# Optimization experiments

Measured on AMD Instinct MI355X. Metric: run time of the kernel, lower is better.

The kernel has to match this reference:

```python
import jax, jax.numpy as jnp
import numpy as np

B, T, HID = 2, 1024, 2048
NH, NKV, HD = 16, 4, 128
L, INTER = 4, 5632
EPS = 1e-6


def _rope_tables(key):
    inv_freq = 1.0 / (10000.0 ** (jnp.arange(0, HD, 2, dtype=jnp.float32) / HD))  # [HD/2]
    pos = jnp.arange(T, dtype=jnp.float32)
    freqs = pos[:, None] * inv_freq[None, :]          # [T, HD/2]
    emb = jnp.concatenate([freqs, freqs], axis=-1)    # [T, HD]
    cos = jnp.broadcast_to(jnp.cos(emb)[None], (B, T, HD))
    sin = jnp.broadcast_to(jnp.sin(emb)[None], (B, T, HD))
    return cos, sin


def setup_inputs() -> dict:
    key = jax.random.key(0)
    ks = jax.random.split(key, 12)
    std = 0.02
    cos, sin = _rope_tables(key)
    return {
        "hidden_states": jax.random.normal(ks[0], (B, T, HID), jnp.float32),
        "cos": cos,
        "sin": sin,
        "qw": jax.random.normal(ks[1], (L, NH * HD, HID), jnp.float32) * std,
        "qb": jnp.zeros((L, NH * HD), jnp.float32),
        "kw": jax.random.normal(ks[2], (L, NKV * HD, HID), jnp.float32) * std,
        "kb": jnp.zeros((L, NKV * HD), jnp.float32),
        "vw": jax.random.normal(ks[3], (L, NKV * HD, HID), jnp.float32) * std,
        "vb": jnp.zeros((L, NKV * HD), jnp.float32),
        "ow": jax.random.normal(ks[4], (L, HID, NH * HD), jnp.float32) * std,
        "gatew": jax.random.normal(ks[5], (L, INTER, HID), jnp.float32) * std,
        "upw": jax.random.normal(ks[6], (L, INTER, HID), jnp.float32) * std,
        "downw": jax.random.normal(ks[7], (L, HID, INTER), jnp.float32) * std,
        "ln1w": jnp.ones((L, HID), jnp.float32),
        "ln2w": jnp.ones((L, HID), jnp.float32),
        "normw": jnp.ones((HID,), jnp.float32),
    }


def _rmsnorm(x, w):
    xf = x.astype(jnp.float32)
    var = jnp.mean(xf * xf, axis=-1, keepdims=True)
    return (w * (xf * jax.lax.rsqrt(var + EPS))).astype(x.dtype)


def _rotate_half(x):
    x1, x2 = x[..., : HD // 2], x[..., HD // 2:]
    return jnp.concatenate([-x2, x1], axis=-1)


def _layer(x, cos, sin, mask, qw, qb, kw, kb, vw, vb, ow, gw, uw, dw, l1, l2):
    # --- attention (PreNorm) ---
    h = _rmsnorm(x, l1)
    q = (h @ qw.T + qb).reshape(B, T, NH, HD).transpose(0, 2, 1, 3)    # [B,NH,T,D]
    k = (h @ kw.T + kb).reshape(B, T, NKV, HD).transpose(0, 2, 1, 3)   # [B,NKV,T,D]
    v = (h @ vw.T + vb).reshape(B, T, NKV, HD).transpose(0, 2, 1, 3)
    c, s = cos[:, None], sin[:, None]                                  # [B,1,T,D]
    q = q * c + _rotate_half(q) * s
    k = k * c + _rotate_half(k) * s
    rep = NH // NKV
    k = jnp.repeat(k, rep, axis=1)                                     # GQA repeat_kv
    v = jnp.repeat(v, rep, axis=1)
    scores = jnp.einsum("bhqd,bhkd->bhqk", q, k) / (HD ** 0.5) + mask
    attn = jax.nn.softmax(scores.astype(jnp.float32), axis=-1).astype(q.dtype)
    ao = jnp.einsum("bhqk,bhkd->bhqd", attn, v)
    ao = ao.transpose(0, 2, 1, 3).reshape(B, T, NH * HD) @ ow.T
    x = x + ao
    # --- SwiGLU MLP (PreNorm) ---
    h = _rmsnorm(x, l2)
    x = x + (jax.nn.silu(h @ gw.T) * (h @ uw.T)) @ dw.T
    return x


def reference(hidden_states, cos, sin, qw, qb, kw, kb, vw, vb, ow,
              gatew, upw, downw, ln1w, ln2w, normw):
    min_val = jnp.finfo(hidden_states.dtype).min
    qpos = jnp.arange(T)
    mask = jnp.where(qpos[None, :] > qpos[:, None], min_val, 0.0).astype(hidden_states.dtype)
    mask = mask[None, None]  # [1,1,T,T]
    x = hidden_states
    for i in range(L):
        x = _layer(x, cos, sin, mask, qw[i], qb[i], kw[i], kb[i], vw[i], vb[i],
                   ow[i], gatew[i], upw[i], downw[i], ln1w[i], ln2w[i])
    return _rmsnorm(x, normw)
```

## Files before the change

kernel.cpp:

```cpp
#include <hip/hip_runtime.h>


typedef __attribute__((ext_vector_type(8))) __bf16 bf16x8;
typedef __attribute__((ext_vector_type(4))) float f32x4;
typedef __attribute__((ext_vector_type(4))) unsigned short u16x4;

#define DEV __device__ __forceinline__
#define BARRIER() asm volatile("s_barrier" ::: "memory")

#define NTOK 2048
#define HIDDIM 2048
#define NHEADS 16
#define NKVH 4
#define HDIM 128
#define KVDIM 512
#define INTERDIM 5632

DEV unsigned short f2bf(float f) {
  union { float f; unsigned u; } a; a.f = f;
  unsigned r = a.u + 0x7fffu + ((a.u >> 16) & 1u);
  return (unsigned short)(r >> 16);
}
DEV float bf2f(unsigned short h) {
  union { unsigned u; float f; } a; a.u = ((unsigned)h) << 16;
  return a.f;
}
DEV unsigned short f2h(float f) {
  union { _Float16 h; unsigned short u; } c; c.h = (_Float16)f; return c.u;
}
DEV float h2f(unsigned short u) {
  union { unsigned short u; _Float16 h; } c; c.u = u; return (float)c.h;
}
DEV void gload_lds16(const void* g, void* l) {
  __builtin_amdgcn_global_load_lds(
      (const __attribute__((address_space(1))) unsigned int*)(g),
      (__attribute__((address_space(3))) unsigned int*)(l), 16, 0, 0);
}

__global__ __launch_bounds__(256) void cvt_kernel(
    const float* __restrict__ in, unsigned short* __restrict__ out, int n8) {
  const int i = blockIdx.x * 256 + threadIdx.x;
  if (i >= n8) return;
  const f32x4* p = reinterpret_cast<const f32x4*>(in) + (size_t)i * 2;
  const f32x4 a = p[0], b = p[1];
  bf16x8 o;
  o[0] = (__bf16)a.x; o[1] = (__bf16)a.y; o[2] = (__bf16)a.z; o[3] = (__bf16)a.w;
  o[4] = (__bf16)b.x; o[5] = (__bf16)b.y; o[6] = (__bf16)b.z; o[7] = (__bf16)b.w;
  *reinterpret_cast<bf16x8*>(out + (size_t)i * 8) = o;
}

__global__ __launch_bounds__(256) void cvt_gu(
    const float* __restrict__ gw, const float* __restrict__ uw,
    unsigned short* __restrict__ out) {
  const int i = blockIdx.x * 256 + threadIdx.x;
  const int row = i >> 8, g8 = i & 255;
  const int t = row >> 8, sub = row & 255;
  const float* src = (sub < 128)
                         ? gw + (size_t)(t * 128 + sub) * 2048
                         : uw + (size_t)(t * 128 + sub - 128) * 2048;
  const f32x4* p = reinterpret_cast<const f32x4*>(src) + (size_t)g8 * 2;
  const f32x4 a = p[0], b = p[1];
  bf16x8 o;
  o[0] = (__bf16)a.x; o[1] = (__bf16)a.y; o[2] = (__bf16)a.z; o[3] = (__bf16)a.w;
  o[4] = (__bf16)b.x; o[5] = (__bf16)b.y; o[6] = (__bf16)b.z; o[7] = (__bf16)b.w;
  *reinterpret_cast<bf16x8*>(out + (size_t)row * 2048 + g8 * 8) = o;
}

template <int OUTF32>
__global__ __launch_bounds__(256) void rmsnorm_kernel(
    const float* __restrict__ x, const float* __restrict__ w,
    void* __restrict__ outp) {
  const int row = blockIdx.x, tid = threadIdx.x;
  const int lane = tid & 63, wave = tid >> 6;
  const float* xr = x + (size_t)row * HIDDIM;
  f32x4 v0 = *reinterpret_cast<const f32x4*>(xr + tid * 4);
  f32x4 v1 = *reinterpret_cast<const f32x4*>(xr + 1024 + tid * 4);
  float ss = v0.x * v0.x + v0.y * v0.y + v0.z * v0.z + v0.w * v0.w +
             v1.x * v1.x + v1.y * v1.y + v1.z * v1.z + v1.w * v1.w;
#pragma unroll
  for (int off = 1; off < 64; off <<= 1) ss += __shfl_xor(ss, off, 64);
  __shared__ float red[4];
  if (lane == 0) red[wave] = ss;
  __syncthreads();
  ss = red[0] + red[1] + red[2] + red[3];
  const float rs = rsqrtf(ss * (1.0f / 2048.0f) + 1e-6f);
  f32x4 w0 = *reinterpret_cast<const f32x4*>(w + tid * 4);
  f32x4 w1 = *reinterpret_cast<const f32x4*>(w + 1024 + tid * 4);
  if (OUTF32) {
    float* o = (float*)outp + (size_t)row * HIDDIM;
    f32x4 o0, o1;
    o0.x = v0.x * rs * w0.x; o0.y = v0.y * rs * w0.y;
    o0.z = v0.z * rs * w0.z; o0.w = v0.w * rs * w0.w;
    o1.x = v1.x * rs * w1.x; o1.y = v1.y * rs * w1.y;
    o1.z = v1.z * rs * w1.z; o1.w = v1.w * rs * w1.w;
    *reinterpret_cast<f32x4*>(o + tid * 4) = o0;
    *reinterpret_cast<f32x4*>(o + 1024 + tid * 4) = o1;
  } else {
    unsigned short* o = (unsigned short*)outp + (size_t)row * HIDDIM;
    u16x4 p0, p1;
    p0.x = f2bf(v0.x * rs * w0.x); p0.y = f2bf(v0.y * rs * w0.y);
    p0.z = f2bf(v0.z * rs * w0.z); p0.w = f2bf(v0.w * rs * w0.w);
    p1.x = f2bf(v1.x * rs * w1.x); p1.y = f2bf(v1.y * rs * w1.y);
    p1.z = f2bf(v1.z * rs * w1.z); p1.w = f2bf(v1.w * rs * w1.w);
    *reinterpret_cast<u16x4*>(o + tid * 4) = p0;
    *reinterpret_cast<u16x4*>(o + 1024 + tid * 4) = p1;
  }
}

template <int KS, int OUTF32>
__global__ __launch_bounds__(256) void reduce_rms(
    float* __restrict__ x, const unsigned short* __restrict__ p, size_t zs,
    const float* __restrict__ w, void* __restrict__ outp) {
  const int row = blockIdx.x, tid = threadIdx.x;
  const int lane = tid & 63, wave = tid >> 6;
  float* xr = x + (size_t)row * HIDDIM;
  f32x4 v0 = *reinterpret_cast<const f32x4*>(xr + tid * 4);
  f32x4 v1 = *reinterpret_cast<const f32x4*>(xr + 1024 + tid * 4);
#pragma unroll
  for (int s = 0; s < KS; ++s) {
    const unsigned short* pr = p + (size_t)s * zs + (size_t)row * HIDDIM;
    u16x4 a = *reinterpret_cast<const u16x4*>(pr + tid * 4);
    u16x4 b = *reinterpret_cast<const u16x4*>(pr + 1024 + tid * 4);
    v0.x += bf2f(a.x); v0.y += bf2f(a.y); v0.z += bf2f(a.z); v0.w += bf2f(a.w);
    v1.x += bf2f(b.x); v1.y += bf2f(b.y); v1.z += bf2f(b.z); v1.w += bf2f(b.w);
  }
  *reinterpret_cast<f32x4*>(xr + tid * 4) = v0;
  *reinterpret_cast<f32x4*>(xr + 1024 + tid * 4) = v1;
  float ss = v0.x * v0.x + v0.y * v0.y + v0.z * v0.z + v0.w * v0.w +
             v1.x * v1.x + v1.y * v1.y + v1.z * v1.z + v1.w * v1.w;
#pragma unroll
  for (int off = 1; off < 64; off <<= 1) ss += __shfl_xor(ss, off, 64);
  __shared__ float red[4];
  if (lane == 0) red[wave] = ss;
  __syncthreads();
  ss = red[0] + red[1] + red[2] + red[3];
  const float rs = rsqrtf(ss * (1.0f / 2048.0f) + 1e-6f);
  f32x4 w0 = *reinterpret_cast<const f32x4*>(w + tid * 4);
  f32x4 w1 = *reinterpret_cast<const f32x4*>(w + 1024 + tid * 4);
  if (OUTF32) {
    float* o = (float*)outp + (size_t)row * HIDDIM;
    f32x4 o0, o1;
    o0.x = v0.x * rs * w0.x; o0.y = v0.y * rs * w0.y;
    o0.z = v0.z * rs * w0.z; o0.w = v0.w * rs * w0.w;
    o1.x = v1.x * rs * w1.x; o1.y = v1.y * rs * w1.y;
    o1.z = v1.z * rs * w1.z; o1.w = v1.w * rs * w1.w;
    *reinterpret_cast<f32x4*>(o + tid * 4) = o0;
    *reinterpret_cast<f32x4*>(o + 1024 + tid * 4) = o1;
  } else {
    unsigned short* o = (unsigned short*)outp + (size_t)row * HIDDIM;
    u16x4 p0, p1;
    p0.x = f2bf(v0.x * rs * w0.x); p0.y = f2bf(v0.y * rs * w0.y);
    p0.z = f2bf(v0.z * rs * w0.z); p0.w = f2bf(v0.w * rs * w0.w);
    p1.x = f2bf(v1.x * rs * w1.x); p1.y = f2bf(v1.y * rs * w1.y);
    p1.z = f2bf(v1.z * rs * w1.z); p1.w = f2bf(v1.w * rs * w1.w);
    *reinterpret_cast<u16x4*>(o + tid * 4) = p0;
    *reinterpret_cast<u16x4*>(o + 1024 + tid * 4) = p1;
  }
}

template <int MB>
DEV void mfma16(const bf16x8 (&aF)[4], const bf16x8 (&bF)[4],
                f32x4 (&acc)[8][4]) {
#pragma unroll
  for (int ni = 0; ni < 4; ++ni)
#pragma unroll
    for (int mi = 0; mi < 4; ++mi)
      acc[MB + mi][ni] = __builtin_amdgcn_mfma_f32_16x16x32_bf16(
          aF[mi], bF[ni], acc[MB + mi][ni], 0, 0, 0);
}

__global__ __launch_bounds__(512, 2) void gemm8p(
    const unsigned short* __restrict__ A, const unsigned short* __restrict__ W,
    unsigned short* __restrict__ outp, int K, int ldo, int kt_split,
    int kt_tot, size_t zstride) {
  __shared__ unsigned short lds[65536];
  const int tid = threadIdx.x, lane = tid & 63, wave = tid >> 6;
  const int fr = lane & 15, lq = lane >> 4;
  const int wm = wave >> 2, wn = wave & 3;

  int bx = blockIdx.x, by = blockIdx.y;
  {
    const int nbx = gridDim.x, nwg = nbx * gridDim.y;
    const int lin = by * nbx + bx, cpx = nwg >> 3;
    const int swz = (lin & 7) * cpx + (lin >> 3);
    bx = swz % nbx; by = swz / nbx;
  }
  const int m0 = by * 256, n0 = bx * 256;
  const int bz = blockIdx.z;
  const int t0 = bz * kt_split;
  int NT = kt_tot - t0; if (NT > kt_split) NT = kt_split;

  const int u0 = tid, u1 = tid + 512;
  const int r0s = u0 >> 3, r1s = u1 >> 3;
  const size_t off0 = (size_t)r0s * K + (size_t)((((u0 & 7) ^ (r0s & 7))) << 3);
  const size_t off1 = (size_t)r1s * K + (size_t)((((u1 & 7) ^ (r1s & 7))) << 3);
  const unsigned short* gb0 = A + (size_t)(m0)*K + (size_t)t0 * 64;
  const unsigned short* gb1 = A + (size_t)(m0 + 128) * K + (size_t)t0 * 64;
  const unsigned short* gb2 = W + (size_t)(n0)*K + (size_t)t0 * 64;
  const unsigned short* gb3 = W + (size_t)(n0 + 128) * K + (size_t)t0 * 64;

#define STAGE(h_, tt_, b_)                                                    \
  do {                                                                        \
    const unsigned short* _g =                                                \
        ((h_) == 0 ? gb0 : (h_) == 1 ? gb1 : (h_) == 2 ? gb2 : gb3) +         \
        (size_t)(tt_)*64;                                                     \
    unsigned short* _l = &lds[(b_)*32768 + (h_)*8192 + wave * 512];           \
    gload_lds16(_g + off0, _l);                                               \
    gload_lds16(_g + off1, _l + 4096);                                        \
  } while (0)

  const int e0 = lq ^ (fr & 7);
  const int cbA = wm * 8192;
  const int cbB = (2 + (wn >> 1)) * 8192;
  const int rB0 = (wn & 1) * 64 + fr;

#define LDA(mi_, ks_, c_)                                                     \
  (*reinterpret_cast<const bf16x8*>(                                          \
      &lds[(c_)*32768 + cbA + ((mi_)*16 + fr) * 64 + ((e0 ^ ((ks_)*4)) << 3)]))
#define LDB(ni_, ks_, c_)                                                     \
  (*reinterpret_cast<const bf16x8*>(                                          \
      &lds[(c_)*32768 + cbB + (rB0 + (ni_)*16) * 64 + ((e0 ^ ((ks_)*4)) << 3)]))

  f32x4 acc[8][4] = {};
  bf16x8 aF[4], bF[4];

  STAGE(0, 0, 0); STAGE(1, 0, 0); STAGE(2, 0, 0); STAGE(3, 0, 0);

  for (int t = 0; t < NT; ++t) {
    const int c = t & 1;
    if (t + 1 < NT) {
      STAGE(0, t + 1, c ^ 1);
      STAGE(2, t + 1, c ^ 1);
      asm volatile("s_waitcnt vmcnt(4)" ::: "memory");
    } else {
      asm volatile("s_waitcnt vmcnt(0)" ::: "memory");
    }
    BARRIER();

    bF[0] = LDB(0, 0, c); bF[1] = LDB(1, 0, c);
    bF[2] = LDB(2, 0, c); bF[3] = LDB(3, 0, c);
    aF[0] = LDA(0, 0, c); aF[1] = LDA(1, 0, c);
    aF[2] = LDA(2, 0, c); aF[3] = LDA(3, 0, c);
    if (t + 1 < NT) { STAGE(1, t + 1, c ^ 1); STAGE(3, t + 1, c ^ 1); }
    BARRIER();
    __builtin_amdgcn_s_setprio(1);
    mfma16<0>(aF, bF, acc);
    __builtin_amdgcn_s_setprio(0);
    __builtin_amdgcn_sched_barrier(0);
    BARRIER();

    aF[0] = LDA(4, 0, c); aF[1] = LDA(5, 0, c);
    aF[2] = LDA(6, 0, c); aF[3] = LDA(7, 0, c);
    BARRIER();
    __builtin_amdgcn_s_setprio(1);
    mfma16<4>(aF, bF, acc);
    __builtin_amdgcn_s_setprio(0);
    __builtin_amdgcn_sched_barrier(0);
    BARRIER();

    bF[0] = LDB(0, 1, c); bF[1] = LDB(1, 1, c);
    bF[2] = LDB(2, 1, c); bF[3] = LDB(3, 1, c);
    aF[0] = LDA(0, 1, c); aF[1] = LDA(1, 1, c);
    aF[2] = LDA(2, 1, c); aF[3] = LDA(3, 1, c);
    BARRIER();
    __builtin_amdgcn_s_setprio(1);
    mfma16<0>(aF, bF, acc);
    __builtin_amdgcn_s_setprio(0);
    __builtin_amdgcn_sched_barrier(0);
    BARRIER();

    aF[0] = LDA(4, 1, c); aF[1] = LDA(5, 1, c);
    aF[2] = LDA(6, 1, c); aF[3] = LDA(7, 1, c);
    BARRIER();
    __builtin_amdgcn_s_setprio(1);
    mfma16<4>(aF, bF, acc);
    __builtin_amdgcn_s_setprio(0);
    __builtin_amdgcn_sched_barrier(0);
    BARRIER();
  }

  const int r0 = lq * 4;
#pragma unroll
  for (int mi = 0; mi < 8; ++mi)
#pragma unroll
    for (int ni = 0; ni < 4; ++ni)
#pragma unroll
      for (int r = 0; r < 4; ++r) {
        const int gm = m0 + wm * 128 + mi * 16 + r0 + r;
        const int gn = n0 + wn * 64 + ni * 16 + fr;
        outp[(size_t)bz * zstride + (size_t)gm * ldo + gn] =
            f2bf(acc[mi][ni][r]);
      }
#undef STAGE
#undef LDA
#undef LDB
}

__global__ __launch_bounds__(512, 2) void gemm_gu(
    const unsigned short* __restrict__ A, const unsigned short* __restrict__ W,
    unsigned short* __restrict__ act) {
  __shared__ unsigned short lds[65536];
  const int tid = threadIdx.x, lane = tid & 63, wave = tid >> 6;
  const int fr = lane & 15, lq = lane >> 4;
  const int wm = wave >> 2, wn = wave & 3;
  const int K = 2048;

  int bx = blockIdx.x, by = blockIdx.y;
  {
    const int nbx = gridDim.x, nwg = nbx * gridDim.y;
    const int lin = by * nbx + bx, cpx = nwg >> 3;
    const int swz = (lin & 7) * cpx + (lin >> 3);
    bx = swz % nbx; by = swz / nbx;
  }
  const int m0 = by * 256, n0 = bx * 256;

  const int u0 = tid, u1 = tid + 512;
  const int r0s = u0 >> 3, r1s = u1 >> 3;
  const size_t off0 = (size_t)r0s * K + (size_t)((((u0 & 7) ^ (r0s & 7))) << 3);
  const size_t off1 = (size_t)r1s * K + (size_t)((((u1 & 7) ^ (r1s & 7))) << 3);
  const unsigned short* gb0 = A + (size_t)(m0)*K;
  const unsigned short* gb1 = A + (size_t)(m0 + 128) * K;
  const unsigned short* gb2 = W + (size_t)(n0)*K;
  const unsigned short* gb3 = W + (size_t)(n0 + 128) * K;

#define STAGE(h_, tt_, b_)                                                    \
  do {                                                                        \
    const unsigned short* _g =                                                \
        ((h_) == 0 ? gb0 : (h_) == 1 ? gb1 : (h_) == 2 ? gb2 : gb3) +         \
        (size_t)(tt_)*64;                                                     \
    unsigned short* _l = &lds[(b_)*32768 + (h_)*8192 + wave * 512];           \
    gload_lds16(_g + off0, _l);                                               \
    gload_lds16(_g + off1, _l + 4096);                                        \
  } while (0)

  const int e0 = lq ^ (fr & 7);
  const int cbA = wm * 8192;
  const int cbB = (2 + (wn >> 1)) * 8192;
  const int rB0 = (wn & 1) * 64 + fr;

#define LDA(mi_, ks_, c_)                                                     \
  (*reinterpret_cast<const bf16x8*>(                                          \
      &lds[(c_)*32768 + cbA + ((mi_)*16 + fr) * 64 + ((e0 ^ ((ks_)*4)) << 3)]))
#define LDB(ni_, ks_, c_)                                                     \
  (*reinterpret_cast<const bf16x8*>(                                          \
      &lds[(c_)*32768 + cbB + (rB0 + (ni_)*16) * 64 + ((e0 ^ ((ks_)*4)) << 3)]))

  f32x4 acc[8][4] = {};
  bf16x8 aF[4], bF[4];

  STAGE(0, 0, 0); STAGE(1, 0, 0); STAGE(2, 0, 0); STAGE(3, 0, 0);

  for (int t = 0; t < 32; ++t) {
    const int c = t & 1;
    if (t + 1 < 32) {
      STAGE(0, t + 1, c ^ 1);
      STAGE(2, t + 1, c ^ 1);
      asm volatile("s_waitcnt vmcnt(4)" ::: "memory");
    } else {
      asm volatile("s_waitcnt vmcnt(0)" ::: "memory");
    }
    BARRIER();
    bF[0] = LDB(0, 0, c); bF[1] = LDB(1, 0, c);
    bF[2] = LDB(2, 0, c); bF[3] = LDB(3, 0, c);
    aF[0] = LDA(0, 0, c); aF[1] = LDA(1, 0, c);
    aF[2] = LDA(2, 0, c); aF[3] = LDA(3, 0, c);
    if (t + 1 < 32) { STAGE(1, t + 1, c ^ 1); STAGE(3, t + 1, c ^ 1); }
    BARRIER();
    __builtin_amdgcn_s_setprio(1);
    mfma16<0>(aF, bF, acc);
    __builtin_amdgcn_s_setprio(0);
    __builtin_amdgcn_sched_barrier(0);
    BARRIER();
    aF[0] = LDA(4, 0, c); aF[1] = LDA(5, 0, c);
    aF[2] = LDA(6, 0, c); aF[3] = LDA(7, 0, c);
    BARRIER();
    __builtin_amdgcn_s_setprio(1);
    mfma16<4>(aF, bF, acc);
    __builtin_amdgcn_s_setprio(0);
    __builtin_amdgcn_sched_barrier(0);
    BARRIER();
    bF[0] = LDB(0, 1, c); bF[1] = LDB(1, 1, c);
    bF[2] = LDB(2, 1, c); bF[3] = LDB(3, 1, c);
    aF[0] = LDA(0, 1, c); aF[1] = LDA(1, 1, c);
    aF[2] = LDA(2, 1, c); aF[3] = LDA(3, 1, c);
    BARRIER();
    __builtin_amdgcn_s_setprio(1);
    mfma16<0>(aF, bF, acc);
    __builtin_amdgcn_s_setprio(0);
    __builtin_amdgcn_sched_barrier(0);
    BARRIER();
    aF[0] = LDA(4, 1, c); aF[1] = LDA(5, 1, c);
    aF[2] = LDA(6, 1, c); aF[3] = LDA(7, 1, c);
    BARRIER();
    __builtin_amdgcn_s_setprio(1);
    mfma16<4>(aF, bF, acc);
    __builtin_amdgcn_s_setprio(0);
    __builtin_amdgcn_sched_barrier(0);
    BARRIER();
  }

  float* fl = reinterpret_cast<float*>(lds);
  const int r0 = lq * 4;
  __syncthreads();
  if (wn < 2) {
#pragma unroll
    for (int mi = 0; mi < 8; ++mi)
#pragma unroll
      for (int ni = 0; ni < 4; ++ni)
#pragma unroll
        for (int r = 0; r < 4; ++r)
          fl[wm * 16384 + (mi * 16 + r0 + r) * 128 + wn * 64 + ni * 16 + fr] =
              acc[mi][ni][r];
  }
  __syncthreads();
  if (wn >= 2) {
    const int wnu = wn - 2;
#pragma unroll
    for (int mi = 0; mi < 8; ++mi)
#pragma unroll
      for (int ni = 0; ni < 4; ++ni)
#pragma unroll
        for (int r = 0; r < 4; ++r) {
          const int mrow = mi * 16 + r0 + r;
          const float g =
              fl[wm * 16384 + mrow * 128 + wnu * 64 + ni * 16 + fr];
          const float s = g / (1.f + __expf(-g));
          const int gm = m0 + wm * 128 + mrow;
          const int ic = (n0 >> 1) + wnu * 64 + ni * 16 + fr;
          act[(size_t)gm * INTERDIM + ic] = f2bf(s * acc[mi][ni][r]);
        }
  }
#undef STAGE
#undef LDA
#undef LDB
}

__global__ __launch_bounds__(512, 2) void gemm_qk(
    const unsigned short* __restrict__ q, const unsigned short* __restrict__ k,
    unsigned short* __restrict__ s) {
  __shared__ unsigned short lds[65536];
  const int tid = threadIdx.x, lane = tid & 63, wave = tid >> 6;
  const int fr = lane & 15, lq = lane >> 4;
  const int wm = wave >> 2, wn = wave & 3;

  int bx = blockIdx.x, by = blockIdx.y;
  {
    const int nbx = gridDim.x, nwg = nbx * gridDim.y;
    const int lin = by * nbx + bx, cpx = nwg >> 3;
    const int swz = (lin & 7) * cpx + (lin >> 3);
    bx = swz % nbx; by = swz / nbx;
  }
  if (bx > by) return;
  const int z = blockIdx.z, b = z >> 4, h = z & 15, kvh = h >> 2;
  const unsigned short* A = q + (size_t)b * 1024 * HIDDIM + h * HDIM;
  const unsigned short* W = k + (size_t)b * 1024 * KVDIM + kvh * HDIM;
  unsigned short* outp = s + (size_t)z * 1048576;
  const int m0 = by * 256, n0 = bx * 256;

  const int u0 = tid, u1 = tid + 512;
  const int r0s = u0 >> 3, r1s = u1 >> 3;
  const int c0 = ((u0 & 7) ^ (r0s & 7)) << 3, c1 = ((u1 & 7) ^ (r1s & 7)) << 3;
  const size_t offA0 = (size_t)r0s * HIDDIM + c0;
  const size_t offA1 = (size_t)r1s * HIDDIM + c1;
  const size_t offW0 = (size_t)r0s * KVDIM + c0;
  const size_t offW1 = (size_t)r1s * KVDIM + c1;
  const unsigned short* gb0 = A + (size_t)m0 * HIDDIM;
  const unsigned short* gb1 = A + (size_t)(m0 + 128) * HIDDIM;
  const unsigned short* gb2 = W + (size_t)n0 * KVDIM;
  const unsigned short* gb3 = W + (size_t)(n0 + 128) * KVDIM;

#define QSTAGE(h_, tt_, b_)                                                   \
  do {                                                                        \
    const unsigned short* _g =                                                \
        ((h_) == 0 ? gb0 : (h_) == 1 ? gb1 : (h_) == 2 ? gb2 : gb3) +         \
        (size_t)(tt_)*64;                                                     \
    const size_t _o0 = (h_) < 2 ? offA0 : offW0;                              \
    const size_t _o1 = (h_) < 2 ? offA1 : offW1;                              \
    unsigned short* _l = &lds[(b_)*32768 + (h_)*8192 + wave * 512];           \
    gload_lds16(_g + _o0, _l);                                                \
    gload_lds16(_g + _o1, _l + 4096);                                         \
  } while (0)

  const int e0 = lq ^ (fr & 7);
  const int cbA = wm * 8192;
  const int cbB = (2 + (wn >> 1)) * 8192;
  const int rB0 = (wn & 1) * 64 + fr;

#define QLDA(mi_, ks_, c_)                                                    \
  (*reinterpret_cast<const bf16x8*>(                                          \
      &lds[(c_)*32768 + cbA + ((mi_)*16 + fr) * 64 + ((e0 ^ ((ks_)*4)) << 3)]))
#define QLDB(ni_, ks_, c_)                                                    \
  (*reinterpret_cast<const bf16x8*>(                                          \
      &lds[(c_)*32768 + cbB + (rB0 + (ni_)*16) * 64 + ((e0 ^ ((ks_)*4)) << 3)]))

  f32x4 acc[8][4] = {};
  bf16x8 aF[4], bF[4];

  QSTAGE(0, 0, 0); QSTAGE(1, 0, 0); QSTAGE(2, 0, 0); QSTAGE(3, 0, 0);

  for (int t = 0; t < 2; ++t) {
    const int c = t & 1;
    if (t == 0) {
      QSTAGE(0, 1, 1); QSTAGE(2, 1, 1);
      asm volatile("s_waitcnt vmcnt(4)" ::: "memory");
    } else {
      asm volatile("s_waitcnt vmcnt(0)" ::: "memory");
    }
    BARRIER();
    bF[0] = QLDB(0, 0, c); bF[1] = QLDB(1, 0, c);
    bF[2] = QLDB(2, 0, c); bF[3] = QLDB(3, 0, c);
    aF[0] = QLDA(0, 0, c); aF[1] = QLDA(1, 0, c);
    aF[2] = QLDA(2, 0, c); aF[3] = QLDA(3, 0, c);
    if (t == 0) { QSTAGE(1, 1, 1); QSTAGE(3, 1, 1); }
    BARRIER();
    __builtin_amdgcn_s_setprio(1);
    mfma16<0>(aF, bF, acc);
    __builtin_amdgcn_s_setprio(0);
    __builtin_amdgcn_sched_barrier(0);
    BARRIER();
    aF[0] = QLDA(4, 0, c); aF[1] = QLDA(5, 0, c);
    aF[2] = QLDA(6, 0, c); aF[3] = QLDA(7, 0, c);
    BARRIER();
    __builtin_amdgcn_s_setprio(1);
    mfma16<4>(aF, bF, acc);
    __builtin_amdgcn_s_setprio(0);
    __builtin_amdgcn_sched_barrier(0);
    BARRIER();
    bF[0] = QLDB(0, 1, c); bF[1] = QLDB(1, 1, c);
    bF[2] = QLDB(2, 1, c); bF[3] = QLDB(3, 1, c);
    aF[0] = QLDA(0, 1, c); aF[1] = QLDA(1, 1, c);
    aF[2] = QLDA(2, 1, c); aF[3] = QLDA(3, 1, c);
    BARRIER();
    __builtin_amdgcn_s_setprio(1);
    mfma16<0>(aF, bF, acc);
    __builtin_amdgcn_s_setprio(0);
    __builtin_amdgcn_sched_barrier(0);
    BARRIER();
    aF[0] = QLDA(4, 1, c); aF[1] = QLDA(5, 1, c);
    aF[2] = QLDA(6, 1, c); aF[3] = QLDA(7, 1, c);
    BARRIER();
    __builtin_amdgcn_s_setprio(1);
    mfma16<4>(aF, bF, acc);
    __builtin_amdgcn_s_setprio(0);
    __builtin_amdgcn_sched_barrier(0);
    BARRIER();
  }

  const float scale = 0.08838834764831845f;
  const int r0 = lq * 4;
#pragma unroll
  for (int mi = 0; mi < 8; ++mi)
#pragma unroll
    for (int ni = 0; ni < 4; ++ni)
#pragma unroll
      for (int r = 0; r < 4; ++r) {
        const int gm = m0 + wm * 128 + mi * 16 + r0 + r;
        const int gn = n0 + wn * 64 + ni * 16 + fr;
        outp[(size_t)gm * 1024 + gn] = f2h(acc[mi][ni][r] * scale);
      }
#undef QSTAGE
#undef QLDA
#undef QLDB
}

__global__ __launch_bounds__(256) void softmax_rows(unsigned short* __restrict__ s) {
  const int row = blockIdx.x, tid = threadIdx.x;
  const int lane = tid & 63, wave = tid >> 6;
  const int qv = row & 1023;
  const int nact = ((qv >> 8) + 1) << 8;
  unsigned short* r = s + (size_t)row * 1024;
  const int col = tid * 4;
  const bool act = (col < nact);
  float v[4];
  if (act) {
    u16x4 raw = *reinterpret_cast<const u16x4*>(r + col);
#pragma unroll
    for (int j = 0; j < 4; ++j)
      v[j] = (col + j <= qv) ? h2f(((unsigned short*)&raw)[j]) : -1e30f;
  } else {
#pragma unroll
    for (int j = 0; j < 4; ++j) v[j] = -1e30f;
  }
  float mx = fmaxf(fmaxf(v[0], v[1]), fmaxf(v[2], v[3]));
#pragma unroll
  for (int off = 1; off < 64; off <<= 1) mx = fmaxf(mx, __shfl_xor(mx, off, 64));
  __shared__ float redm[4], reds[4];
  if (lane == 0) redm[wave] = mx;
  __syncthreads();
  const float M = fmaxf(fmaxf(redm[0], redm[1]), fmaxf(redm[2], redm[3]));
  float e[4], ts = 0.f;
#pragma unroll
  for (int j = 0; j < 4; ++j) {
    e[j] = (act && col + j <= qv) ? __expf(v[j] - M) : 0.f;
    ts += e[j];
  }
#pragma unroll
  for (int off = 1; off < 64; off <<= 1) ts += __shfl_xor(ts, off, 64);
  if (lane == 0) reds[wave] = ts;
  __syncthreads();
  const float inv = 1.f / (reds[0] + reds[1] + reds[2] + reds[3]);
  if (act) {
    u16x4 o;
    o.x = f2bf(e[0] * inv); o.y = f2bf(e[1] * inv);
    o.z = f2bf(e[2] * inv); o.w = f2bf(e[3] * inv);
    *reinterpret_cast<u16x4*>(r + col) = o;
  }
}

__global__ __launch_bounds__(256, 2) void gemm_pv(
    const unsigned short* __restrict__ p, const unsigned short* __restrict__ vt,
    unsigned short* __restrict__ ao) {
  __shared__ unsigned short lds[40960];
  const int tid = threadIdx.x, lane = tid & 63, wave = tid >> 6;
  const int fr = lane & 15, lq = lane >> 4;
  const int bxn = blockIdx.x, by = blockIdx.y, z = blockIdx.z;
  const int b = z >> 4, h = z & 15, kvh = h >> 2;
  const int m0p = by * 256, n0 = bxn * 64;
  const int NT = by * 4 + 4;

  const unsigned short* A = p + (size_t)z * 1048576 + (size_t)m0p * 1024;
  const unsigned short* W =
      vt + ((size_t)(b * 4 + kvh) * 128 + n0) * 1024;

#define PVSTAGE(tt_, c_)                                                      \
  do {                                                                        \
    _Pragma("unroll")                                                         \
    for (int j = 0; j < 8; ++j) {                                             \
      const int u = wave * 512 + j * 64 + lane;                               \
      const int rw = u >> 3;                                                  \
      gload_lds16(A + (size_t)rw * 1024 + (((u & 7) ^ (rw & 7)) << 3) +       \
                      (size_t)(tt_)*64,                                       \
                  &lds[(c_)*20480 + wave * 4096 + j * 512]);                  \
    }                                                                         \
    _Pragma("unroll")                                                         \
    for (int j = 0; j < 2; ++j) {                                             \
      const int u = wave * 128 + j * 64 + lane;                               \
      const int rw = u >> 3;                                                  \
      gload_lds16(W + (size_t)rw * 1024 + (((u & 7) ^ (rw & 7)) << 3) +       \
                      (size_t)(tt_)*64,                                       \
                  &lds[(c_)*20480 + 16384 + wave * 1024 + j * 512]);          \
    }                                                                         \
  } while (0)

  const int e0 = lq ^ (fr & 7);
#define PVLDA(mi_, ks_, c_)                                                   \
  (*reinterpret_cast<const bf16x8*>(                                          \
      &lds[(c_)*20480 + (wave * 64 + (mi_)*16 + fr) * 64 +                    \
           ((e0 ^ ((ks_)*4)) << 3)]))
#define PVLDB(ni_, ks_, c_)                                                   \
  (*reinterpret_cast<const bf16x8*>(                                          \
      &lds[(c_)*20480 + 16384 + ((ni_)*16 + fr) * 64 +                        \
           ((e0 ^ ((ks_)*4)) << 3)]))

  f32x4 acc[4][4] = {};
  bf16x8 aF[4], bF[4];

  PVSTAGE(0, 0);

  for (int t = 0; t < NT; ++t) {
    const int c = t & 1;
    if (t + 1 < NT) {
      PVSTAGE(t + 1, c ^ 1);
      asm volatile("s_waitcnt vmcnt(10)" ::: "memory");
    } else {
      asm volatile("s_waitcnt vmcnt(0)" ::: "memory");
    }
    BARRIER();
#pragma unroll
    for (int ks = 0; ks < 2; ++ks) {
      bF[0] = PVLDB(0, ks, c); bF[1] = PVLDB(1, ks, c);
      bF[2] = PVLDB(2, ks, c); bF[3] = PVLDB(3, ks, c);
      aF[0] = PVLDA(0, ks, c); aF[1] = PVLDA(1, ks, c);
      aF[2] = PVLDA(2, ks, c); aF[3] = PVLDA(3, ks, c);
      BARRIER();
      __builtin_amdgcn_s_setprio(1);
#pragma unroll
      for (int ni = 0; ni < 4; ++ni)
#pragma unroll
        for (int mi = 0; mi < 4; ++mi)
          acc[mi][ni] = __builtin_amdgcn_mfma_f32_16x16x32_bf16(
              aF[mi], bF[ni], acc[mi][ni], 0, 0, 0);
      __builtin_amdgcn_s_setprio(0);
      __builtin_amdgcn_sched_barrier(0);
      BARRIER();
    }
  }

  const int r0 = lq * 4;
#pragma unroll
  for (int mi = 0; mi < 4; ++mi)
#pragma unroll
    for (int ni = 0; ni < 4; ++ni)
#pragma unroll
      for (int r = 0; r < 4; ++r) {
        const int gm = m0p + wave * 64 + mi * 16 + r0 + r;
        const int gn = n0 + ni * 16 + fr;
        ao[(size_t)(b * 1024 + gm) * HIDDIM + h * HDIM + gn] =
            f2bf(acc[mi][ni][r]);
      }
#undef PVSTAGE
#undef PVLDA
#undef PVLDB
}

__global__ __launch_bounds__(256) void reduce_qkv(
    const unsigned short* __restrict__ p, const float* __restrict__ qb,
    const float* __restrict__ kb, const float* __restrict__ vb,
    const float* __restrict__ cosb, const float* __restrict__ sinb,
    unsigned short* __restrict__ qo, unsigned short* __restrict__ ko,
    unsigned short* __restrict__ vto) {
  const int i = blockIdx.x * 256 + threadIdx.x;
  const int row = i / 768, c4 = (i - row * 768) * 4;
  const unsigned short* p0 = p + (size_t)row * 3072;
  const unsigned short* p1 = p + 6291456 + (size_t)row * 3072;
  const u16x4 a0 = *reinterpret_cast<const u16x4*>(p0 + c4);
  const u16x4 a1 = *reinterpret_cast<const u16x4*>(p1 + c4);
  f32x4 s;
  s.x = bf2f(a0.x) + bf2f(a1.x); s.y = bf2f(a0.y) + bf2f(a1.y);
  s.z = bf2f(a0.z) + bf2f(a1.z); s.w = bf2f(a0.w) + bf2f(a1.w);
  if (c4 < 2560) {
    const float* bias; unsigned short* out; int d, ldo;
    if (c4 < 2048) { bias = qb; out = qo; d = c4;        ldo = HIDDIM; }
    else           { bias = kb; out = ko; d = c4 - 2048; ldo = KVDIM; }
    const int dd = d & 127;
    const bool lohalf = (dd < 64);
    const int pc = lohalf ? c4 + 64 : c4 - 64;
    const int pd = lohalf ? d + 64 : d - 64;
    const u16x4 b0 = *reinterpret_cast<const u16x4*>(p0 + pc);
    const u16x4 b1 = *reinterpret_cast<const u16x4*>(p1 + pc);
    f32x4 sp;
    sp.x = bf2f(b0.x) + bf2f(b1.x); sp.y = bf2f(b0.y) + bf2f(b1.y);
    sp.z = bf2f(b0.z) + bf2f(b1.z); sp.w = bf2f(b0.w) + bf2f(b1.w);
    const f32x4 bv = *reinterpret_cast<const f32x4*>(bias + d);
    const f32x4 bp = *reinterpret_cast<const f32x4*>(bias + pd);
    const f32x4 cv = *reinterpret_cast<const f32x4*>(cosb + (size_t)row * 128 + dd);
    const f32x4 sv = *reinterpret_cast<const f32x4*>(sinb + (size_t)row * 128 + dd);
    const f32x4 xv = s + bv, pv = sp + bp;
    f32x4 o;
    if (lohalf) o = xv * cv - pv * sv;
    else        o = xv * cv + pv * sv;
    u16x4 ob;
    ob.x = f2bf(o.x); ob.y = f2bf(o.y); ob.z = f2bf(o.z); ob.w = f2bf(o.w);
    *reinterpret_cast<u16x4*>(out + (size_t)row * ldo + d) = ob;
  } else {
    const int d = c4 - 2560;
    const int kvh = d >> 7, dd = d & 127;
    const int b = row >> 10, t = row & 1023;
    const f32x4 bv = *reinterpret_cast<const f32x4*>(vb + d);
    const f32x4 o = s + bv;
    unsigned short* vr =
        vto + ((size_t)(b * 4 + kvh) * 128 + dd) * 1024 + t;
    vr[0] = f2bf(o.x); vr[1024] = f2bf(o.y);
    vr[2048] = f2bf(o.z); vr[3072] = f2bf(o.w);
  }
}

extern "C" void kernel_launch(void* const* d_in, const int* in_sizes, int n_in,
                              void* d_out, int out_size, void* d_ws,
                              size_t ws_size, hipStream_t stream) {
  (void)in_sizes; (void)n_in; (void)out_size; (void)ws_size;
  const float* hidden = (const float*)d_in[0];
  const float* cosb  = (const float*)d_in[1];
  const float* sinb  = (const float*)d_in[2];
  const float* qw    = (const float*)d_in[3];
  const float* qbias = (const float*)d_in[4];
  const float* kw    = (const float*)d_in[5];
  const float* kbias = (const float*)d_in[6];
  const float* vw    = (const float*)d_in[7];
  const float* vbias = (const float*)d_in[8];
  const float* ow    = (const float*)d_in[9];
  const float* gw    = (const float*)d_in[10];
  const float* uw    = (const float*)d_in[11];
  const float* dw    = (const float*)d_in[12];
  const float* ln1   = (const float*)d_in[13];
  const float* ln2   = (const float*)d_in[14];
  const float* normw = (const float*)d_in[15];

  char* ws = (char*)d_ws;
  float* x               = (float*)ws;
  unsigned short* hbuf   = (unsigned short*)(ws + 16777216);
  unsigned short* qbuf   = (unsigned short*)(ws + 25165824);
  unsigned short* kbuf   = (unsigned short*)(ws + 33554432);
  unsigned short* vtbuf  = (unsigned short*)(ws + 35651584);
  unsigned short* aobuf  = (unsigned short*)(ws + 39845888);
  unsigned short* actbuf = (unsigned short*)(ws + 71303168);
  unsigned short* wcvt   = (unsigned short*)(ws + 94371840);
  unsigned short* pbQKV = (unsigned short*)(ws + 37748736);
  unsigned short* sbuf = (unsigned short*)(ws + 48234496);
  unsigned short* pbO = (unsigned short*)(ws + 48234496);
  unsigned short* wgu = (unsigned short*)(ws + 25165824);
  unsigned short* pbD = (unsigned short*)(ws + 25165824);

  unsigned short* wq16 = wcvt;
  unsigned short* wk16 = wcvt + 4194304;
  unsigned short* wv16 = wcvt + 5242880;
  unsigned short* ow16 = wcvt;

  hipMemcpyAsync(x, hidden, (size_t)NTOK * HIDDIM * 4,
                 hipMemcpyDeviceToDevice, stream);
  rmsnorm_kernel<0><<<NTOK, 256, 0, stream>>>(x, ln1, hbuf);

  for (int l = 0; l < 4; ++l) {
    const float* qw_l = qw + (size_t)l * 2048 * 2048;
    const float* qb_l = qbias + (size_t)l * 2048;
    const float* kw_l = kw + (size_t)l * 512 * 2048;
    const float* kb_l = kbias + (size_t)l * 512;
    const float* vw_l = vw + (size_t)l * 512 * 2048;
    const float* vb_l = vbias + (size_t)l * 512;
    const float* ow_l = ow + (size_t)l * 2048 * 2048;
    const float* gw_l = gw + (size_t)l * 5632 * 2048;
    const float* uw_l = uw + (size_t)l * 5632 * 2048;
    const float* dw_l = dw + (size_t)l * 2048 * 5632;

    cvt_kernel<<<2048, 256, 0, stream>>>(qw_l, wq16, 524288);
    cvt_kernel<<<512, 256, 0, stream>>>(kw_l, wk16, 131072);
    cvt_kernel<<<512, 256, 0, stream>>>(vw_l, wv16, 131072);
    gemm8p<<<dim3(12, 8, 2), 512, 0, stream>>>(
        hbuf, wcvt, pbQKV, 2048, 3072, 16, 32, (size_t)6291456);
    reduce_qkv<<<6144, 256, 0, stream>>>(pbQKV, qb_l, kb_l, vb_l, cosb, sinb,
                                         qbuf, kbuf, vtbuf);

    gemm_qk<<<dim3(4, 4, 32), 512, 0, stream>>>(qbuf, kbuf, sbuf);
    softmax_rows<<<32768, 256, 0, stream>>>(sbuf);
    gemm_pv<<<dim3(2, 4, 32), 256, 0, stream>>>(sbuf, vtbuf, aobuf);

    cvt_kernel<<<2048, 256, 0, stream>>>(ow_l, ow16, 524288);
    gemm8p<<<dim3(8, 8, 2), 512, 0, stream>>>(
        aobuf, ow16, pbO, 2048, 2048, 16, 32, (size_t)4194304);
    reduce_rms<2, 0><<<NTOK, 256, 0, stream>>>(x, pbO, (size_t)4194304,
                                               ln2 + l * 2048, hbuf);

    cvt_gu<<<11264, 256, 0, stream>>>(gw_l, uw_l, wgu);
    gemm_gu<<<dim3(44, 8), 512, 0, stream>>>(hbuf, wgu, actbuf);

    cvt_kernel<<<5632, 256, 0, stream>>>(dw_l, wcvt, 1441792);
    gemm8p<<<dim3(8, 8, 3), 512, 0, stream>>>(
        actbuf, wcvt, pbD, 5632, 2048, 30, 88, (size_t)4194304);
    if (l < 3) {
      reduce_rms<3, 0><<<NTOK, 256, 0, stream>>>(
          x, pbD, (size_t)4194304, ln1 + (l + 1) * 2048, hbuf);
    } else {
      reduce_rms<3, 1><<<NTOK, 256, 0, stream>>>(x, pbD, (size_t)4194304,
                                                 normw, d_out);
    }
  }
}
```

Before: 1.695 ms.

## Restructure GEMMs into 16-wave blocks with 64x64 wave tiles and K-step 32

Replaces the 8-wave GEMM kernels, which used 128x64 wave tiles, K-step 64, XOR-swizzled LDS and a 128KB double buffer, with 1024-thread kernels. In the new kernels each of 16 waves computes a 64x64 tile, using a single K-step of 32 and a 64KB unswizzled double buffer. The fused gate/up epilogue now stages each wave row in turn through the smaller LDS. Split-K factors also change: the O projection and down projection move to 4-way split, with matching reduce kernels. The aim is more latency hiding from more waves per tile and less LDS per block, at the cost of lower per-wave register reuse, more barriers per unit of work and more split-K partial traffic.

```diff
diff --git a/kernel.cpp b/kernel.cpp
--- a/kernel.cpp
+++ b/kernel.cpp
@@ -10,10 +10,8 @@
 
 #define NTOK 2048
 #define HIDDIM 2048
-#define NHEADS 16
-#define NKVH 4
+#define KVDIM 512
 #define HDIM 128
-#define KVDIM 512
 #define INTERDIM 5632
 
 DEV unsigned short f2bf(float f) {
@@ -158,22 +156,75 @@
   }
 }
 
-template <int MB>
-DEV void mfma16(const bf16x8 (&aF)[4], const bf16x8 (&bF)[4],
-                f32x4 (&acc)[8][4]) {
-#pragma unroll
-  for (int ni = 0; ni < 4; ++ni)
-#pragma unroll
-    for (int mi = 0; mi < 4; ++mi)
-      acc[MB + mi][ni] = __builtin_amdgcn_mfma_f32_16x16x32_bf16(
-          aF[mi], bF[ni], acc[MB + mi][ni], 0, 0, 0);
-}
-
-__global__ __launch_bounds__(512, 2) void gemm8p(
+struct G16Setup {
+  const unsigned short* srcp0;
+  const unsigned short* srcp1;
+  int ldsc0, ldsc1;
+};
+
+DEV G16Setup g16_setup(const unsigned short* A, const unsigned short* W,
+                       int K, int m0, int n0, int t0, int wave, int lane) {
+  const int c0 = wave * 2, c1 = wave * 2 + 1;
+  const int rA = lane >> 2, cg = (lane & 3) * 8;
+  G16Setup s;
+  const unsigned short* gb[4] = {
+      A + (size_t)m0 * K, A + (size_t)(m0 + 128) * K,
+      W + (size_t)n0 * K, W + (size_t)(n0 + 128) * K};
+  s.srcp0 = gb[c0 >> 3] + (size_t)((c0 & 7) * 16 + rA) * K + cg +
+            (size_t)t0 * 32;
+  s.srcp1 = gb[c1 >> 3] + (size_t)((c1 & 7) * 16 + rA) * K + cg +
+            (size_t)t0 * 32;
+  s.ldsc0 = c0 * 512;
+  s.ldsc1 = c1 * 512;
+  return s;
+}
+
+#define G16STAGE(st_, tt_, c_)                                                \
+  do {                                                                        \
+    gload_lds16(st_.srcp0 + (size_t)(tt_)*32, &lds[(c_)*16384 + st_.ldsc0]);  \
+    gload_lds16(st_.srcp1 + (size_t)(tt_)*32, &lds[(c_)*16384 + st_.ldsc1]);  \
+  } while (0)
+
+#define G16LDA(mi_, c_)                                                       \
+  (*reinterpret_cast<const bf16x8*>(                                          \
+      &lds[(c_)*16384 + (wm >> 1) * 4096 +                                    \
+           (((wm & 1) * 64) + (mi_)*16 + fr) * 32 + lq * 8]))
+#define G16LDB(ni_, c_)                                                       \
+  (*reinterpret_cast<const bf16x8*>(                                          \
+      &lds[(c_)*16384 + (2 + (wn >> 1)) * 4096 +                              \
+           (((wn & 1) * 64) + (ni_)*16 + fr) * 32 + lq * 8]))
+
+#define G16KLOOP(NT_)                                                         \
+  G16STAGE(st, 0, 0);                                                         \
+  for (int t = 0; t < (NT_); ++t) {                                           \
+    const int c = t & 1;                                                      \
+    if (t + 1 < (NT_)) {                                                      \
+      G16STAGE(st, t + 1, c ^ 1);                                             \
+      asm volatile("s_waitcnt vmcnt(2)" ::: "memory");                        \
+    } else {                                                                  \
+      asm volatile("s_waitcnt vmcnt(0)" ::: "memory");                        \
+    }                                                                         \
+    BARRIER();                                                                \
+    bf16x8 aF[4], bF[4];                                                      \
+    bF[0] = G16LDB(0, c); bF[1] = G16LDB(1, c);                               \
+    bF[2] = G16LDB(2, c); bF[3] = G16LDB(3, c);                               \
+    aF[0] = G16LDA(0, c); aF[1] = G16LDA(1, c);                               \
+    aF[2] = G16LDA(2, c); aF[3] = G16LDA(3, c);                               \
+    __builtin_amdgcn_s_setprio(1);                                            \
+    _Pragma("unroll") for (int ni = 0; ni < 4; ++ni)                          \
+        _Pragma("unroll") for (int mi = 0; mi < 4; ++mi)                      \
+            acc[mi][ni] = __builtin_amdgcn_mfma_f32_16x16x32_bf16(            \
+                aF[mi], bF[ni], acc[mi][ni], 0, 0, 0);                        \
+    __builtin_amdgcn_s_setprio(0);                                            \
+    __builtin_amdgcn_sched_barrier(0);                                        \
+    BARRIER();                                                                \
+  }
+
+__global__ __launch_bounds__(1024) void gemm16w(
     const unsigned short* __restrict__ A, const unsigned short* __restrict__ W,
     unsigned short* __restrict__ outp, int K, int ldo, int kt_split,
     int kt_tot, size_t zstride) {
-  __shared__ unsigned short lds[65536];
+  __shared__ unsigned short lds[32768];
   const int tid = threadIdx.x, lane = tid & 63, wave = tid >> 6;
   const int fr = lane & 15, lq = lane >> 4;
   const int wm = wave >> 2, wn = wave & 3;
@@ -190,116 +241,28 @@
   const int t0 = bz * kt_split;
   int NT = kt_tot - t0; if (NT > kt_split) NT = kt_split;
 
-  const int u0 = tid, u1 = tid + 512;
-  const int r0s = u0 >> 3, r1s = u1 >> 3;
-  const size_t off0 = (size_t)r0s * K + (size_t)((((u0 & 7) ^ (r0s & 7))) << 3);
-  const size_t off1 = (size_t)r1s * K + (size_t)((((u1 & 7) ^ (r1s & 7))) << 3);
-  const unsigned short* gb0 = A + (size_t)(m0)*K + (size_t)t0 * 64;
-  const unsigned short* gb1 = A + (size_t)(m0 + 128) * K + (size_t)t0 * 64;
-  const unsigned short* gb2 = W + (size_t)(n0)*K + (size_t)t0 * 64;
-  const unsigned short* gb3 = W + (size_t)(n0 + 128) * K + (size_t)t0 * 64;
-
-#define STAGE(h_, tt_, b_)                                                    \
-  do {                                                                        \
-    const unsigned short* _g =                                                \
-        ((h_) == 0 ? gb0 : (h_) == 1 ? gb1 : (h_) == 2 ? gb2 : gb3) +         \
-        (size_t)(tt_)*64;                                                     \
-    unsigned short* _l = &lds[(b_)*32768 + (h_)*8192 + wave * 512];           \
-    gload_lds16(_g + off0, _l);                                               \
-    gload_lds16(_g + off1, _l + 4096);                                        \
-  } while (0)
-
-  const int e0 = lq ^ (fr & 7);
-  const int cbA = wm * 8192;
-  const int cbB = (2 + (wn >> 1)) * 8192;
-  const int rB0 = (wn & 1) * 64 + fr;
-
-#define LDA(mi_, ks_, c_)                                                     \
-  (*reinterpret_cast<const bf16x8*>(                                          \
-      &lds[(c_)*32768 + cbA + ((mi_)*16 + fr) * 64 + ((e0 ^ ((ks_)*4)) << 3)]))
-#define LDB(ni_, ks_, c_)                                                     \
-  (*reinterpret_cast<const bf16x8*>(                                          \
-      &lds[(c_)*32768 + cbB + (rB0 + (ni_)*16) * 64 + ((e0 ^ ((ks_)*4)) << 3)]))
-
-  f32x4 acc[8][4] = {};
-  bf16x8 aF[4], bF[4];
-
-  STAGE(0, 0, 0); STAGE(1, 0, 0); STAGE(2, 0, 0); STAGE(3, 0, 0);
-
-  for (int t = 0; t < NT; ++t) {
-    const int c = t & 1;
-    if (t + 1 < NT) {
-      STAGE(0, t + 1, c ^ 1);
-      STAGE(2, t + 1, c ^ 1);
-      asm volatile("s_waitcnt vmcnt(4)" ::: "memory");
-    } else {
-      asm volatile("s_waitcnt vmcnt(0)" ::: "memory");
-    }
-    BARRIER();
-
-    bF[0] = LDB(0, 0, c); bF[1] = LDB(1, 0, c);
-    bF[2] = LDB(2, 0, c); bF[3] = LDB(3, 0, c);
-    aF[0] = LDA(0, 0, c); aF[1] = LDA(1, 0, c);
-    aF[2] = LDA(2, 0, c); aF[3] = LDA(3, 0, c);
-    if (t + 1 < NT) { STAGE(1, t + 1, c ^ 1); STAGE(3, t + 1, c ^ 1); }
-    BARRIER();
-    __builtin_amdgcn_s_setprio(1);
-    mfma16<0>(aF, bF, acc);
-    __builtin_amdgcn_s_setprio(0);
-    __builtin_amdgcn_sched_barrier(0);
-    BARRIER();
-
-    aF[0] = LDA(4, 0, c); aF[1] = LDA(5, 0, c);
-    aF[2] = LDA(6, 0, c); aF[3] = LDA(7, 0, c);
-    BARRIER();
-    __builtin_amdgcn_s_setprio(1);
-    mfma16<4>(aF, bF, acc);
-    __builtin_amdgcn_s_setprio(0);
-    __builtin_amdgcn_sched_barrier(0);
-    BARRIER();
-
-    bF[0] = LDB(0, 1, c); bF[1] = LDB(1, 1, c);
-    bF[2] = LDB(2, 1, c); bF[3] = LDB(3, 1, c);
-    aF[0] = LDA(0, 1, c); aF[1] = LDA(1, 1, c);
-    aF[2] = LDA(2, 1, c); aF[3] = LDA(3, 1, c);
-    BARRIER();
-    __builtin_amdgcn_s_setprio(1);
-    mfma16<0>(aF, bF, acc);
-    __builtin_amdgcn_s_setprio(0);
-    __builtin_amdgcn_sched_barrier(0);
-    BARRIER();
-
-    aF[0] = LDA(4, 1, c); aF[1] = LDA(5, 1, c);
-    aF[2] = LDA(6, 1, c); aF[3] = LDA(7, 1, c);
-    BARRIER();
-    __builtin_amdgcn_s_setprio(1);
-    mfma16<4>(aF, bF, acc);
-    __builtin_amdgcn_s_setprio(0);
-    __builtin_amdgcn_sched_barrier(0);
-    BARRIER();
-  }
+  G16Setup st = g16_setup(A, W, K, m0, n0, t0, wave, lane);
+  f32x4 acc[4][4] = {};
+  G16KLOOP(NT);
 
   const int r0 = lq * 4;
 #pragma unroll
-  for (int mi = 0; mi < 8; ++mi)
+  for (int mi = 0; mi < 4; ++mi)
 #pragma unroll
     for (int ni = 0; ni < 4; ++ni)
 #pragma unroll
       for (int r = 0; r < 4; ++r) {
-        const int gm = m0 + wm * 128 + mi * 16 + r0 + r;
+        const int gm = m0 + wm * 64 + mi * 16 + r0 + r;
         const int gn = n0 + wn * 64 + ni * 16 + fr;
         outp[(size_t)bz * zstride + (size_t)gm * ldo + gn] =
             f2bf(acc[mi][ni][r]);
       }
-#undef STAGE
-#undef LDA
-#undef LDB
-}
-
-__global__ __launch_bounds__(512, 2) void gemm_gu(
+}
+
+__global__ __launch_bounds__(1024) void gemm_gu16(
     const unsigned short* __restrict__ A, const unsigned short* __restrict__ W,
     unsigned short* __restrict__ act) {
-  __shared__ unsigned short lds[65536];
+  __shared__ unsigned short lds[32768];
   const int tid = threadIdx.x, lane = tid & 63, wave = tid >> 6;
   const int fr = lane & 15, lq = lane >> 4;
   const int wm = wave >> 2, wn = wave & 3;
@@ -314,125 +277,54 @@
   }
   const int m0 = by * 256, n0 = bx * 256;
 
-  const int u0 = tid, u1 = tid + 512;
-  const int r0s = u0 >> 3, r1s = u1 >> 3;
-  const size_t off0 = (size_t)r0s * K + (size_t)((((u0 & 7) ^ (r0s & 7))) << 3);
-  const size_t off1 = (size_t)r1s * K + (size_t)((((u1 & 7) ^ (r1s & 7))) << 3);
-  const unsigned short* gb0 = A + (size_t)(m0)*K;
-  const unsigned short* gb1 = A + (size_t)(m0 + 128) * K;
-  const unsigned short* gb2 = W + (size_t)(n0)*K;
-  const unsigned short* gb3 = W + (size_t)(n0 + 128) * K;
-
-#define STAGE(h_, tt_, b_)                                                    \
-  do {                                                                        \
-    const unsigned short* _g =                                                \
-        ((h_) == 0 ? gb0 : (h_) == 1 ? gb1 : (h_) == 2 ? gb2 : gb3) +         \
-        (size_t)(tt_)*64;                                                     \
-    unsigned short* _l = &lds[(b_)*32768 + (h_)*8192 + wave * 512];           \
-    gload_lds16(_g + off0, _l);                                               \
-    gload_lds16(_g + off1, _l + 4096);                                        \
-  } while (0)
-
-  const int e0 = lq ^ (fr & 7);
-  const int cbA = wm * 8192;
-  const int cbB = (2 + (wn >> 1)) * 8192;
-  const int rB0 = (wn & 1) * 64 + fr;
-
-#define LDA(mi_, ks_, c_)                                                     \
-  (*reinterpret_cast<const bf16x8*>(                                          \
-      &lds[(c_)*32768 + cbA + ((mi_)*16 + fr) * 64 + ((e0 ^ ((ks_)*4)) << 3)]))
-#define LDB(ni_, ks_, c_)                                                     \
-  (*reinterpret_cast<const bf16x8*>(                                          \
-      &lds[(c_)*32768 + cbB + (rB0 + (ni_)*16) * 64 + ((e0 ^ ((ks_)*4)) << 3)]))
-
-  f32x4 acc[8][4] = {};
-  bf16x8 aF[4], bF[4];
-
-  STAGE(0, 0, 0); STAGE(1, 0, 0); STAGE(2, 0, 0); STAGE(3, 0, 0);
-
-  for (int t = 0; t < 32; ++t) {
-    const int c = t & 1;
-    if (t + 1 < 32) {
-      STAGE(0, t + 1, c ^ 1);
-      STAGE(2, t + 1, c ^ 1);
-      asm volatile("s_waitcnt vmcnt(4)" ::: "memory");
-    } else {
-      asm volatile("s_waitcnt vmcnt(0)" ::: "memory");
-    }
-    BARRIER();
-    bF[0] = LDB(0, 0, c); bF[1] = LDB(1, 0, c);
-    bF[2] = LDB(2, 0, c); bF[3] = LDB(3, 0, c);
-    aF[0] = LDA(0, 0, c); aF[1] = LDA(1, 0, c);
-    aF[2] = LDA(2, 0, c); aF[3] = LDA(3, 0, c);
-    if (t + 1 < 32) { STAGE(1, t + 1, c ^ 1); STAGE(3, t + 1, c ^ 1); }
-    BARRIER();
-    __builtin_amdgcn_s_setprio(1);
-    mfma16<0>(aF, bF, acc);
-    __builtin_amdgcn_s_setprio(0);
-    __builtin_amdgcn_sched_barrier(0);
-    BARRIER();
-    aF[0] = LDA(4, 0, c); aF[1] = LDA(5, 0, c);
-    aF[2] = LDA(6, 0, c); aF[3] = LDA(7, 0, c);
-    BARRIER();
-    __builtin_amdgcn_s_setprio(1);
-    mfma16<4>(aF, bF, acc);
-    __builtin_amdgcn_s_setprio(0);
-    __builtin_amdgcn_sched_barrier(0);
-    BARRIER();
-    bF[0] = LDB(0, 1, c); bF[1] = LDB(1, 1, c);
-    bF[2] = LDB(2, 1, c); bF[3] = LDB(3, 1, c);
-    aF[0] = LDA(0, 1, c); aF[1] = LDA(1, 1, c);
-    aF[2] = LDA(2, 1, c); aF[3] = LDA(3, 1, c);
-    BARRIER();
-    __builtin_amdgcn_s_setprio(1);
-    mfma16<0>(aF, bF, acc);
-    __builtin_amdgcn_s_setprio(0);
-    __builtin_amdgcn_sched_barrier(0);
-    BARRIER();
-    aF[0] = LDA(4, 1, c); aF[1] = LDA(5, 1, c);
-    aF[2] = LDA(6, 1, c); aF[3] = LDA(7, 1, c);
-    BARRIER();
-    __builtin_amdgcn_s_setprio(1);
-    mfma16<4>(aF, bF, acc);
-    __builtin_amdgcn_s_setprio(0);
-    __builtin_amdgcn_sched_barrier(0);
-    BARRIER();
-  }
+  G16Setup st = g16_setup(A, W, K, m0, n0, 0, wave, lane);
+  f32x4 acc[4][4] = {};
+  G16KLOOP(64);
 
   float* fl = reinterpret_cast<float*>(lds);
   const int r0 = lq * 4;
-  __syncthreads();
-  if (wn < 2) {
-#pragma unroll
-    for (int mi = 0; mi < 8; ++mi)
-#pragma unroll
-      for (int ni = 0; ni < 4; ++ni)
-#pragma unroll
-        for (int r = 0; r < 4; ++r)
-          fl[wm * 16384 + (mi * 16 + r0 + r) * 128 + wn * 64 + ni * 16 + fr] =
-              acc[mi][ni][r];
-  }
-  __syncthreads();
-  if (wn >= 2) {
-    const int wnu = wn - 2;
-#pragma unroll
-    for (int mi = 0; mi < 8; ++mi)
-#pragma unroll
-      for (int ni = 0; ni < 4; ++ni)
-#pragma unroll
-        for (int r = 0; r < 4; ++r) {
-          const int mrow = mi * 16 + r0 + r;
-          const float g =
-              fl[wm * 16384 + mrow * 128 + wnu * 64 + ni * 16 + fr];
-          const float s = g / (1.f + __expf(-g));
-          const int gm = m0 + wm * 128 + mrow;
-          const int ic = (n0 >> 1) + wnu * 64 + ni * 16 + fr;
-          act[(size_t)gm * INTERDIM + ic] = f2bf(s * acc[mi][ni][r]);
-        }
-  }
-#undef STAGE
-#undef LDA
-#undef LDB
+#pragma unroll 1
+  for (int rd = 0; rd < 4; ++rd) {
+    __syncthreads();
+    if (wm == rd && wn < 2) {
+#pragma unroll
+      for (int mi = 0; mi < 4; ++mi)
+#pragma unroll
+        for (int ni = 0; ni < 4; ++ni)
+#pragma unroll
+          for (int r = 0; r < 4; ++r)
+            fl[(mi * 16 + r0 + r) * 128 + wn * 64 + ni * 16 + fr] =
+                acc[mi][ni][r];
+    }
+    __syncthreads();
+    if (wm == rd && wn >= 2) {
+      const int wnu = wn - 2;
+#pragma unroll
+      for (int mi = 0; mi < 4; ++mi)
+#pragma unroll
+        for (int ni = 0; ni < 4; ++ni)
+#pragma unroll
+          for (int r = 0; r < 4; ++r) {
+            const int mrow = mi * 16 + r0 + r;
+            const float g = fl[mrow * 128 + wnu * 64 + ni * 16 + fr];
+            const float s = g / (1.f + __expf(-g));
+            const int gm = m0 + wm * 64 + mrow;
+            const int ic = (n0 >> 1) + wnu * 64 + ni * 16 + fr;
+            act[(size_t)gm * INTERDIM + ic] = f2bf(s * acc[mi][ni][r]);
+          }
+    }
+  }
+}
+
+template <int MB>
+DEV void mfma16(const bf16x8 (&aF)[4], const bf16x8 (&bF)[4],
+                f32x4 (&acc)[8][4]) {
+#pragma unroll
+  for (int ni = 0; ni < 4; ++ni)
+#pragma unroll
+    for (int mi = 0; mi < 4; ++mi)
+      acc[MB + mi][ni] = __builtin_amdgcn_mfma_f32_16x16x32_bf16(
+          aF[mi], bF[ni], acc[MB + mi][ni], 0, 0, 0);
 }
 
 __global__ __launch_bounds__(512, 2) void gemm_qk(
@@ -786,10 +678,10 @@
   unsigned short* actbuf = (unsigned short*)(ws + 71303168);
   unsigned short* wcvt   = (unsigned short*)(ws + 94371840);
   unsigned short* pbQKV = (unsigned short*)(ws + 37748736);
-  unsigned short* sbuf = (unsigned short*)(ws + 48234496);
-  unsigned short* pbO = (unsigned short*)(ws + 48234496);
-  unsigned short* wgu = (unsigned short*)(ws + 25165824);
-  unsigned short* pbD = (unsigned short*)(ws + 25165824);
+  unsigned short* sbuf  = (unsigned short*)(ws + 48234496);
+  unsigned short* pbO   = (unsigned short*)(ws + 48234496);
+  unsigned short* wgu   = (unsigned short*)(ws + 25165824);
+  unsigned short* pbD   = (unsigned short*)(ws + 25165824);
 
   unsigned short* wq16 = wcvt;
   unsigned short* wk16 = wcvt + 4194304;
@@ -815,8 +707,8 @@
     cvt_kernel<<<2048, 256, 0, stream>>>(qw_l, wq16, 524288);
     cvt_kernel<<<512, 256, 0, stream>>>(kw_l, wk16, 131072);
     cvt_kernel<<<512, 256, 0, stream>>>(vw_l, wv16, 131072);
-    gemm8p<<<dim3(12, 8, 2), 512, 0, stream>>>(
-        hbuf, wcvt, pbQKV, 2048, 3072, 16, 32, (size_t)6291456);
+    gemm16w<<<dim3(12, 8, 2), 1024, 0, stream>>>(
+        hbuf, wcvt, pbQKV, 2048, 3072, 32, 64, (size_t)6291456);
     reduce_qkv<<<6144, 256, 0, stream>>>(pbQKV, qb_l, kb_l, vb_l, cosb, sinb,
                                          qbuf, kbuf, vtbuf);
 
@@ -825,22 +717,22 @@
     gemm_pv<<<dim3(2, 4, 32), 256, 0, stream>>>(sbuf, vtbuf, aobuf);
 
     cvt_kernel<<<2048, 256, 0, stream>>>(ow_l, ow16, 524288);
-    gemm8p<<<dim3(8, 8, 2), 512, 0, stream>>>(
-        aobuf, ow16, pbO, 2048, 2048, 16, 32, (size_t)4194304);
-    reduce_rms<2, 0><<<NTOK, 256, 0, stream>>>(x, pbO, (size_t)4194304,
+    gemm16w<<<dim3(8, 8, 4), 1024, 0, stream>>>(
+        aobuf, ow16, pbO, 2048, 2048, 16, 64, (size_t)4194304);
+    reduce_rms<4, 0><<<NTOK, 256, 0, stream>>>(x, pbO, (size_t)4194304,
                                                ln2 + l * 2048, hbuf);
 
     cvt_gu<<<11264, 256, 0, stream>>>(gw_l, uw_l, wgu);
-    gemm_gu<<<dim3(44, 8), 512, 0, stream>>>(hbuf, wgu, actbuf);
+    gemm_gu16<<<dim3(44, 8), 1024, 0, stream>>>(hbuf, wgu, actbuf);
 
     cvt_kernel<<<5632, 256, 0, stream>>>(dw_l, wcvt, 1441792);
-    gemm8p<<<dim3(8, 8, 3), 512, 0, stream>>>(
-        actbuf, wcvt, pbD, 5632, 2048, 30, 88, (size_t)4194304);
+    gemm16w<<<dim3(8, 8, 4), 1024, 0, stream>>>(
+        actbuf, wcvt, pbD, 5632, 2048, 44, 176, (size_t)4194304);
     if (l < 3) {
-      reduce_rms<3, 0><<<NTOK, 256, 0, stream>>>(
+      reduce_rms<4, 0><<<NTOK, 256, 0, stream>>>(
           x, pbD, (size_t)4194304, ln1 + (l + 1) * 2048, hbuf);
     } else {
-      reduce_rms<3, 1><<<NTOK, 256, 0, stream>>>(x, pbD, (size_t)4194304,
+      reduce_rms<4, 1><<<NTOK, 256, 0, stream>>>(x, pbD, (size_t)4194304,
                                                  normw, d_out);
     }
   }
```

Result: no change. 1.710 ms (+0.9%).
